# Optimization experiments

Measured on AMD Instinct MI355X. Metric: run time of the kernel, lower is better.

Reference implementation:

```python
import jax, jax.numpy as jnp
import numpy as np

N, E = 100000, 1600000
EPS = 1e-5  # BatchNorm1d default eps


def setup_inputs() -> dict:
    key = jax.random.key(0)
    ks = jax.random.split(key, 12)
    rn = lambda k, s, sc=0.05: jax.random.normal(k, s, dtype=jnp.float32) * sc
    return {
        "x": rn(ks[0], (N, 4), 1.0),
        "edge_attr": rn(ks[1], (E, 1), 1.0),
        "edge_index": jax.random.randint(ks[2], (2, E), 0, N),
        # Meta1 edge model: NNConv(9 -> 84) acting as a per-edge linear, + BN(84)
        "W_e1": rn(ks[3], (9, 84)), "b_e1": jnp.zeros((84,), jnp.float32),
        "g_bn1": jnp.ones((84,), jnp.float32), "be_bn1": jnp.zeros((84,), jnp.float32),
        # Meta1 node model: NNConv(88 -> 128) + BN(128), then Linear(132, 64)
        "W_n1": rn(ks[4], (88, 128)), "b_n1": jnp.zeros((128,), jnp.float32),
        "g_bn2": jnp.ones((128,), jnp.float32), "be_bn2": jnp.zeros((128,), jnp.float32),
        "W_m2": rn(ks[5], (132, 64)), "b_m2": jnp.zeros((64,), jnp.float32),
        # Meta2 edge model: Linear(212, 1)
        "W_e2": rn(ks[6], (212, 1)), "b_e2": jnp.zeros((1,), jnp.float32),
        # Meta2 node model: Linear(65, 4) (output discarded by the module)
        "W_n2": rn(ks[7], (65, 4)), "b_n2": jnp.zeros((4,), jnp.float32),
    }


def _batchnorm(h, g, b):
    # training-mode BatchNorm1d: batch mean / biased batch var
    m = jnp.mean(h, axis=0)
    v = jnp.mean(jnp.square(h - m), axis=0)
    return (h - m) * jax.lax.rsqrt(v + EPS) * g + b


def _scatter_mean(vals, idx, n):
    s = jax.ops.segment_sum(vals, idx, num_segments=n)
    cnt = jax.ops.segment_sum(jnp.ones((vals.shape[0],), vals.dtype), idx, num_segments=n)
    return s / jnp.maximum(cnt, 1.0)[:, None]


def reference(x, edge_attr, edge_index, W_e1, b_e1, g_bn1, be_bn1,
              W_n1, b_n1, g_bn2, be_bn2, W_m2, b_m2, W_e2, b_e2, W_n2, b_n2):
    row, col = edge_index[0], edge_index[1]
    n = x.shape[0]
    # --- Meta layer 1 ---
    # edge model: cat([src, dest, edge_attr]) -> NNConv(9,84) -> BN(84)
    e_in = jnp.concatenate([x[row], x[col], edge_attr], axis=1)            # [E, 9]
    e1 = _batchnorm(e_in @ W_e1 + b_e1, g_bn1, be_bn1)                     # [E, 84]
    # node model 1: gather + linear + BN + scatter_mean + concat + MLP
    h = jnp.concatenate([x[col], e1], axis=1) @ W_n1 + b_n1                # [E, 128]
    h = _batchnorm(h, g_bn2, be_bn2)
    agg = _scatter_mean(h, row, n)                                         # [N, 128]
    x1 = jax.nn.relu(jnp.concatenate([x, agg], axis=1) @ W_m2 + b_m2)      # [N, 64]
    # --- Meta layer 2 ---
    e2 = jax.nn.relu(
        jnp.concatenate([x1[row], x1[col], e1], axis=1) @ W_e2 + b_e2)     # [E, 1]
    # node model 2 is computed by the torch module but its output is discarded
    h2 = jax.nn.relu(jnp.concatenate([x1[col], e2], axis=1) @ W_n2 + b_n2)  # [E, 4]
    _x2 = jnp.concatenate([x1, _scatter_mean(h2, row, n)], axis=1)         # dead code
    return e2
```

## Files before the change

### kernel.cpp

```cpp
#include <hip/hip_runtime.h>


#define NBLK_A 512
#define CAPB 24
#define SHIFTB 7
#define SUBB 128
#define STGCAP 2048
#define M21 0x1FFFFFULL
#define QS2 2048.0f
#define QB2 16384

__global__ __launch_bounds__(1024) void k_passA(
    const int* __restrict__ ei, const float* __restrict__ ea,
    int2* __restrict__ rec, int* __restrict__ len,
    int NB, int E, int EPB)
{
    __shared__ int hist[1024];
    int t = threadIdx.x;
    int blk = blockIdx.x;
    if (t < 1024) hist[t] = 0;
    __syncthreads();
    int e0 = blk * EPB;
    int e1 = min(E, e0 + EPB);
    size_t base = (size_t)blk * NB;
    for (int e = e0 + t; e < e1; e += 1024) {
        int r = ei[e];
        int c = ei[E + e];
        float a = ea[e];
        int b = r >> SHIFTB;
        int slot = atomicAdd(&hist[b], 1);
        if (slot < CAPB) {
            int w0 = c | ((r & (SUBB - 1)) << 17);
            rec[(base + b) * CAPB + slot] = make_int2(w0, __float_as_int(a));
        }
    }
    __syncthreads();
    if (t < NB) len[base + t] = min(hist[t], CAPB);
}

__global__ __launch_bounds__(256) void k_passBR(
    const int2* __restrict__ rec, const int* __restrict__ len,
    const float4* __restrict__ x4, float* __restrict__ MSx,
    float* __restrict__ Tp, float* __restrict__ Up, int N, int NB)
{
    __shared__ unsigned long long Sacc[SUBB * 2];
    __shared__ int pre[257];
    __shared__ int wtot[4];
    __shared__ int2 stg[STGCAP];
    __shared__ float redT[40];
    __shared__ float redU[16];
    int t = threadIdx.x;
    int b = blockIdx.x;
    int w = t >> 6;
    int lane = t & 63;
    for (int k = t; k < SUBB * 2; k += 256) Sacc[k] = 0ULL;
    if (t < 40) redT[t] = 0.f;
    if (t < 16) redU[t] = 0.f;
    float u[15];
#pragma unroll
    for (int k = 0; k < 15; ++k) u[k] = 0.f;
    __syncthreads();
#pragma unroll
    for (int r = 0; r < NBLK_A / 256; ++r) {
        int seg = r * 256 + t;
        int lv = min(len[(size_t)seg * NB + b], CAPB);
        int v = lv;
#pragma unroll
        for (int off = 1; off < 64; off <<= 1) {
            int s = __shfl_up(v, off);
            if (lane >= off) v += s;
        }
        if (lane == 63) wtot[w] = v;
        __syncthreads();
        int wadd = 0;
#pragma unroll
        for (int k = 0; k < 4; ++k)
            if (k < w) wadd += wtot[k];
        pre[t + 1] = v + wadd;
        if (t == 0) pre[0] = 0;
        __syncthreads();
        int R = min(pre[256], STGCAP);
        int beg = pre[t + 1] - lv;
        const int2* sp = &rec[((size_t)seg * NB + b) * CAPB];
        for (int i = 0; i < lv; ++i) {
            int d = beg + i;
            if (d < STGCAP) stg[d] = sp[i];
        }
        __syncthreads();
#pragma unroll 4
        for (int idx = t; idx < R; idx += 256) {
            int2 v2 = stg[idx];
            int c = v2.x & 0x1FFFF;
            int ridx = v2.x >> 17;
            float a = __int_as_float(v2.y);
            float4 xc = x4[c];
            int q0 = __float2int_rn(xc.x * QS2);
            int q1 = __float2int_rn(xc.y * QS2);
            int q2 = __float2int_rn(xc.z * QS2);
            int q3 = __float2int_rn(xc.w * QS2);
            int qa = __float2int_rn(a * QS2);
            q0 = min(max(q0, -16383), 16383);
            q1 = min(max(q1, -16383), 16383);
            q2 = min(max(q2, -16383), 16383);
            q3 = min(max(q3, -16383), 16383);
            qa = min(max(qa, -16383), 16383);
            unsigned long long w0 =
                (unsigned long long)(unsigned)(q0 + QB2) |
                ((unsigned long long)(unsigned)(q1 + QB2) << 21) |
                ((unsigned long long)(unsigned)(q2 + QB2) << 42);
            unsigned long long w1 =
                (unsigned long long)(unsigned)(q3 + QB2) |
                ((unsigned long long)(unsigned)(qa + QB2) << 21) |
                (1ULL << 42);
            atomicAdd(&Sacc[ridx * 2], w0);
            atomicAdd(&Sacc[ridx * 2 + 1], w1);
            float zc[4] = {xc.x, xc.y, xc.z, xc.w};
            int q = 0;
#pragma unroll
            for (int i = 0; i < 4; ++i)
#pragma unroll
                for (int k = i; k < 4; ++k) { u[q] = fmaf(zc[i], zc[k], u[q]); ++q; }
#pragma unroll
            for (int i = 0; i < 4; ++i) u[10 + i] = fmaf(zc[i], a, u[10 + i]);
            u[14] = fmaf(a, a, u[14]);
        }
        __syncthreads();
    }
    float Tacc[39];
#pragma unroll
    for (int k = 0; k < 39; ++k) Tacc[k] = 0.f;
    int n = b * SUBB + t;
    if (t < SUBB && n < N) {
        unsigned long long w0 = Sacc[t * 2];
        unsigned long long w1 = Sacc[t * 2 + 1];
        long long f0 = (long long)(w0 & M21);
        long long f1 = (long long)((w0 >> 21) & M21);
        long long f2 = (long long)((w0 >> 42) & M21);
        long long f3 = (long long)(w1 & M21);
        long long fa = (long long)((w1 >> 21) & M21);
        long long cn = (long long)(w1 >> 42);
        float cnt = (float)cn;
        long long bias = cn * (long long)QB2;
        float S[6];
        S[0] = (float)(f0 - bias) / QS2;
        S[1] = (float)(f1 - bias) / QS2;
        S[2] = (float)(f2 - bias) / QS2;
        S[3] = (float)(f3 - bias) / QS2;
        S[4] = (float)(fa - bias) / QS2;
        S[5] = cnt;
        float4 xn = x4[n];
        float x[4] = {xn.x, xn.y, xn.z, xn.w};
        int q = 0;
#pragma unroll
        for (int a = 0; a < 4; ++a)
#pragma unroll
            for (int bb = a; bb < 4; ++bb) { Tacc[q] = cnt * x[a] * x[bb]; ++q; }
#pragma unroll
        for (int a = 0; a < 4; ++a)
#pragma unroll
            for (int bb = 0; bb < 4; ++bb) Tacc[10 + a * 4 + bb] = x[a] * S[bb];
#pragma unroll
        for (int a = 0; a < 4; ++a) {
            Tacc[26 + a] = x[a] * S[4];
            Tacc[30 + a] = cnt * x[a];
            Tacc[34 + a] = S[a];
        }
        Tacc[38] = S[4];
        float inv = cnt > 0.f ? 1.f / cnt : 0.f;
        float4* m = (float4*)(MSx + (size_t)n * 8);
        m[0] = make_float4(S[0] * inv, S[1] * inv, S[2] * inv, S[3] * inv);
        m[1] = make_float4(S[4] * inv, cnt > 0.f ? 1.f : 0.f, 0.f, 0.f);
    }
#pragma unroll
    for (int v = 0; v < 39; ++v) {
        float s = Tacc[v];
#pragma unroll
        for (int off = 32; off > 0; off >>= 1) s += __shfl_down(s, off);
        if (lane == 0) atomicAdd(&redT[v], s);
    }
#pragma unroll
    for (int v = 0; v < 15; ++v) {
        float s = u[v];
#pragma unroll
        for (int off = 32; off > 0; off >>= 1) s += __shfl_down(s, off);
        if (lane == 0) atomicAdd(&redU[v], s);
    }
    __syncthreads();
    if (t < 39) Tp[(size_t)b * 40 + t] = redT[t];
    else if (t >= 64 && t < 79) Up[(size_t)b * 16 + (t - 64)] = redU[t - 64];
}

__device__ __forceinline__ int sym4(int a, int b) {
    return a * 4 - a * (a - 1) / 2 + (b - a);
}

__global__ __launch_bounds__(1024) void k_setup(
    const float* __restrict__ Up, const float* __restrict__ Tp,
    int NBu, int NTb,
    const float* __restrict__ We1, const float* __restrict__ be1,
    const float* __restrict__ g1, const float* __restrict__ bb1,
    const float* __restrict__ Wn1, const float* __restrict__ bn1,
    const float* __restrict__ g2, const float* __restrict__ bb2,
    const float* __restrict__ We2, const float* __restrict__ be2,
    const float* __restrict__ Wm2, const float* __restrict__ bm2,
    float* __restrict__ G, float* __restrict__ c0g, float* __restrict__ kvg,
    int E)
{
    __shared__ float ZCl[64];
    __shared__ float Zf[100];
    __shared__ float s1[84], sh1[84];
    __shared__ float Ml[10 * 128];
    __shared__ float s2l[128], sh2l[128];
    __shared__ float Ep[16 * 64 * 11];
    __shared__ float We1l[9 * 84];
    __shared__ __align__(16) float Wn1l[88 * 128];
    __shared__ __align__(16) float Wm2l[132 * 64];
    __shared__ float We2l[212];
    __shared__ float be1l[84], g1l[84], bb1l[84];
    __shared__ float bn1l[128], g2l[128], bb2l[128];
    __shared__ float bm2l[64], be2l[1];
    int t = threadIdx.x;
    int lane = t & 63;
    if (t < 64) ZCl[t] = 0.f;
    {
        const float4* s4 = (const float4*)Wn1;
        float4* d4 = (float4*)Wn1l;
        for (int i = t; i < 88 * 128 / 4; i += 1024) d4[i] = s4[i];
        const float4* s5 = (const float4*)Wm2;
        float4* d5 = (float4*)Wm2l;
        for (int i = t; i < 132 * 64 / 4; i += 1024) d5[i] = s5[i];
        for (int i = t; i < 9 * 84; i += 1024) We1l[i] = We1[i];
        if (t < 212) We2l[t] = We2[t];
        if (t < 84) { be1l[t] = be1[t]; g1l[t] = g1[t]; bb1l[t] = bb1[t]; }
        else if (t >= 128 && t < 256) {
            int i = t - 128;
            bn1l[i] = bn1[i]; g2l[i] = g2[i]; bb2l[i] = bb2[i];
        } else if (t >= 256 && t < 320) bm2l[t - 256] = bm2[t - 256];
        if (t == 320) be2l[0] = be2[0];
    }
    float us[15];
#pragma unroll
    for (int k = 0; k < 15; ++k) us[k] = 0.f;
    for (int i = t; i < NBu; i += 1024)
#pragma unroll
        for (int k = 0; k < 15; ++k) us[k] += Up[(size_t)i * 16 + k];
    float ts[39];
#pragma unroll
    for (int k = 0; k < 39; ++k) ts[k] = 0.f;
    for (int i = t; i < NTb; i += 1024)
#pragma unroll
        for (int k = 0; k < 39; ++k) ts[k] += Tp[(size_t)i * 40 + k];
    __syncthreads();
#pragma unroll
    for (int v = 0; v < 15; ++v) {
        float s = us[v];
#pragma unroll
        for (int off = 32; off > 0; off >>= 1) s += __shfl_down(s, off);
        if (lane == 0) atomicAdd(&ZCl[39 + v], s);
    }
#pragma unroll
    for (int v = 0; v < 39; ++v) {
        float s = ts[v];
#pragma unroll
        for (int off = 32; off > 0; off >>= 1) s += __shfl_down(s, off);
        if (lane == 0) atomicAdd(&ZCl[v], s);
    }
    __syncthreads();
    if (t < 100) {
        int i = t / 10, jj = t % 10;
        int a_ = i < jj ? i : jj;
        int b_ = i < jj ? jj : i;
        float v;
        if (b_ < 4) v = ZCl[sym4(a_, b_)];
        else if (b_ < 8) {
            if (a_ < 4) v = ZCl[10 + a_ * 4 + (b_ - 4)];
            else v = ZCl[39 + sym4(a_ - 4, b_ - 4)];
        } else if (b_ == 8) {
            if (a_ < 4) v = ZCl[26 + a_];
            else if (a_ < 8) v = ZCl[49 + (a_ - 4)];
            else v = ZCl[53];
        } else {
            if (a_ < 4) v = ZCl[30 + a_];
            else if (a_ < 8) v = ZCl[34 + (a_ - 4)];
            else if (a_ == 8) v = ZCl[38];
            else v = (float)E;
        }
        Zf[t] = v;
    }
    __syncthreads();
    float Ef = (float)E;
    if (t < 84) {
        float w[10];
#pragma unroll
        for (int i = 0; i < 9; ++i) w[i] = We1l[i * 84 + t];
        w[9] = be1l[t];
        float sm = 0.f, sq = 0.f;
#pragma unroll
        for (int i = 0; i < 10; ++i) {
            sm += Zf[90 + i] * w[i];
            float zi = 0.f;
#pragma unroll
            for (int jj = 0; jj < 10; ++jj) zi += Zf[i * 10 + jj] * w[jj];
            sq += w[i] * zi;
        }
        float m = sm / Ef;
        float var = sq / Ef - m * m;
        float sc = g1l[t] * rsqrtf(var + 1e-5f);
        s1[t] = sc;
        sh1[t] = bb1l[t] - m * sc;
    }
    __syncthreads();
    {
        int j = t & 127;
        int sub = t >> 7;
        float col[10];
#pragma unroll
        for (int i = 0; i < 10; ++i) col[i] = 0.f;
        int k0 = sub * 11;
        int k1 = min(84, k0 + 11);
        for (int k = k0; k < k1; ++k) {
            float wn = Wn1l[(4 + k) * 128 + j];
            float ws_ = s1[k] * wn;
#pragma unroll
            for (int i = 0; i < 9; ++i) col[i] = fmaf(We1l[i * 84 + k], ws_, col[i]);
            col[9] += be1l[k] * ws_ + sh1[k] * wn;
        }
        float* bp = &Ep[(size_t)(sub * 128 + j) * 10];
#pragma unroll
        for (int i = 0; i < 10; ++i) bp[i] = col[i];
    }
    __syncthreads();
    if (t < 128) {
        float col[10];
#pragma unroll
        for (int i = 0; i < 10; ++i) col[i] = 0.f;
        for (int sub = 0; sub < 8; ++sub) {
            const float* bp = &Ep[(size_t)(sub * 128 + t) * 10];
#pragma unroll
            for (int i = 0; i < 10; ++i) col[i] += bp[i];
        }
#pragma unroll
        for (int i = 0; i < 4; ++i) col[4 + i] += Wn1l[i * 128 + t];
        col[9] += bn1l[t];
#pragma unroll
        for (int i = 0; i < 10; ++i) Ml[i * 128 + t] = col[i];
    }
    __syncthreads();
    if (t < 128) {
        float col[10];
#pragma unroll
        for (int i = 0; i < 10; ++i) col[i] = Ml[i * 128 + t];
        float sm = 0.f, sq = 0.f;
#pragma unroll
        for (int i = 0; i < 10; ++i) {
            sm += Zf[90 + i] * col[i];
            float zi = 0.f;
#pragma unroll
            for (int jj = 0; jj < 10; ++jj) zi += Zf[i * 10 + jj] * col[jj];
            sq += col[i] * zi;
        }
        float m = sm / Ef;
        float var = sq / Ef - m * m;
        float sc = g2l[t] * rsqrtf(var + 1e-5f);
        s2l[t] = sc;
        sh2l[t] = bb2l[t] - m * sc;
    } else if (t >= 128 && t < 768) {
        int col = (t - 128) >> 6;
        float kv = 0.f;
        if (col < 9) {
            for (int k = lane; k < 84; k += 64)
                kv = fmaf(We1l[col * 84 + k] * s1[k], We2l[128 + k], kv);
        } else {
            for (int k = lane; k < 84; k += 64)
                kv = fmaf(be1l[k] * s1[k] + sh1[k], We2l[128 + k], kv);
        }
#pragma unroll
        for (int off = 32; off > 0; off >>= 1) kv += __shfl_down(kv, off);
        if (lane == 0) kvg[col] = kv + (col == 9 ? be2l[0] : 0.f);
    }
    __syncthreads();
    {
        int j = t & 63;
        int sub = t >> 6;
        float gcol[10];
#pragma unroll
        for (int i = 0; i < 10; ++i) gcol[i] = 0.f;
        float c0 = 0.f;
        int k0 = sub * 8;
        for (int k = k0; k < k0 + 8; ++k) {
            float bkj = Wm2l[(4 + k) * 64 + j];
            float m = s2l[k] * bkj;
#pragma unroll
            for (int i = 0; i < 10; ++i) gcol[i] = fmaf(Ml[i * 128 + k], m, gcol[i]);
            c0 = fmaf(sh2l[k], bkj, c0);
        }
        float* ep = &Ep[(size_t)(sub * 64 + j) * 11];
#pragma unroll
        for (int i = 0; i < 10; ++i) ep[i] = gcol[i];
        ep[10] = c0;
    }
    __syncthreads();
    if (t < 64) {
        float gcol[10];
#pragma unroll
        for (int i = 0; i < 10; ++i) gcol[i] = 0.f;
        float c0 = 0.f;
        for (int sub = 0; sub < 16; ++sub) {
            const float* ep = &Ep[(size_t)(sub * 64 + t) * 11];
#pragma unroll
            for (int i = 0; i < 10; ++i) gcol[i] += ep[i];
            c0 += ep[10];
        }
#pragma unroll
        for (int i = 0; i < 4; ++i) gcol[i] += Wm2l[i * 64 + t];
        c0 += bm2l[t];
#pragma unroll
        for (int i = 0; i < 10; ++i) G[i * 64 + t] = gcol[i];
        c0g[t] = c0;
    }
}

__global__ __launch_bounds__(256) void k_nodesB(
    const float4* __restrict__ x4, const float* __restrict__ MSx,
    const float* __restrict__ G, const float* __restrict__ c0g,
    const float* __restrict__ kv, const float* __restrict__ Wm2,
    const float* __restrict__ bm2, const float* __restrict__ We2,
    float* __restrict__ P, float* __restrict__ Q, int N)
{
    __shared__ float Gl[640], c0l[64], Al[256], bl[64], ul[64], vl[64], kvl[10];
    int t = threadIdx.x;
    for (int k = t; k < 640; k += 256) Gl[k] = G[k];
    if (t < 64) {
        c0l[t] = c0g[t];
        bl[t] = bm2[t];
        ul[t] = We2[t];
        vl[t] = We2[64 + t];
    }
    for (int k = t; k < 256; k += 256) Al[k] = Wm2[k];
    if (t < 10) kvl[t] = kv[t];
    __syncthreads();
    int n = blockIdx.x * 256 + t;
    if (n >= N) return;
    float4 xn = x4[n];
    const float4* m = (const float4*)(MSx + (size_t)n * 8);
    float4 m0 = m[0];
    float4 m1 = m[1];
    bool has = m1.y > 0.5f;
    float Pv = 0.f, Qv = 0.f;
    if (has) {
        float zb[10] = {xn.x, xn.y, xn.z, xn.w, m0.x, m0.y, m0.z, m0.w, m1.x, 1.f};
#pragma unroll 4
        for (int j = 0; j < 64; ++j) {
            float s = c0l[j];
#pragma unroll
            for (int i = 0; i < 10; ++i) s = fmaf(zb[i], Gl[i * 64 + j], s);
            s = fmaxf(s, 0.f);
            Pv = fmaf(s, ul[j], Pv);
            Qv = fmaf(s, vl[j], Qv);
        }
    } else {
#pragma unroll 4
        for (int j = 0; j < 64; ++j) {
            float s = bl[j] + xn.x * Al[j] + xn.y * Al[64 + j] +
                      xn.z * Al[128 + j] + xn.w * Al[192 + j];
            s = fmaxf(s, 0.f);
            Pv = fmaf(s, ul[j], Pv);
            Qv = fmaf(s, vl[j], Qv);
        }
    }
    P[n] = Pv + xn.x * kvl[0] + xn.y * kvl[1] + xn.z * kvl[2] + xn.w * kvl[3];
    Q[n] = Qv + xn.x * kvl[4] + xn.y * kvl[5] + xn.z * kvl[6] + xn.w * kvl[7];
}

__global__ __launch_bounds__(256) void k_edges_out(
    const int* __restrict__ ei, const float* __restrict__ ea,
    const float* __restrict__ P, const float* __restrict__ Q,
    const float* __restrict__ kv, float* __restrict__ out, int E)
{
    int e4 = blockIdx.x * 256 + threadIdx.x;
    int e = e4 * 4;
    float k8 = kv[8], k9 = kv[9];
    if (e + 3 < E) {
        int4 rr = *(const int4*)&ei[e];
        int4 cc = *(const int4*)&ei[E + e];
        float4 aa = *(const float4*)&ea[e];
        float4 o;
        o.x = fmaxf(P[rr.x] + Q[cc.x] + aa.x * k8 + k9, 0.f);
        o.y = fmaxf(P[rr.y] + Q[cc.y] + aa.y * k8 + k9, 0.f);
        o.z = fmaxf(P[rr.z] + Q[cc.z] + aa.z * k8 + k9, 0.f);
        o.w = fmaxf(P[rr.w] + Q[cc.w] + aa.w * k8 + k9, 0.f);
        *(float4*)&out[e] = o;
    } else {
        for (; e < E; ++e) {
            float s = P[ei[e]] + Q[ei[E + e]] + ea[e] * k8 + k9;
            out[e] = fmaxf(s, 0.f);
        }
    }
}

extern "C" void kernel_launch(void* const* d_in, const int* in_sizes, int n_in,
                              void* d_out, int out_size, void* d_ws, size_t ws_size,
                              hipStream_t stream)
{
    const float* x   = (const float*)d_in[0];
    const float* ea  = (const float*)d_in[1];
    const int*   ei  = (const int*)d_in[2];
    const float* We1 = (const float*)d_in[3];
    const float* be1 = (const float*)d_in[4];
    const float* g1  = (const float*)d_in[5];
    const float* bb1 = (const float*)d_in[6];
    const float* Wn1 = (const float*)d_in[7];
    const float* bn1 = (const float*)d_in[8];
    const float* g2  = (const float*)d_in[9];
    const float* bb2 = (const float*)d_in[10];
    const float* Wm2 = (const float*)d_in[11];
    const float* bm2 = (const float*)d_in[12];
    const float* We2 = (const float*)d_in[13];
    const float* be2 = (const float*)d_in[14];

    int N = in_sizes[0] / 4;
    int E = in_sizes[1];
    int EPB = (E + NBLK_A - 1) / NBLK_A;

    int NB = (N + SUBB - 1) >> SHIFTB;

    float* ws  = (float*)d_ws;
    float* G   = ws + 64;
    float* c0  = ws + 704;
    float* kv  = ws + 768;
    float* P   = ws + 1024;
    float* Q   = P + N;
    float* MSx = Q + N;
    int*   len = (int*)(MSx + 8 * (size_t)N);
    int2*  rec = (int2*)(len + (size_t)NBLK_A * NB);

    float* Up = P;
    float* Tp = P + 32768;

    k_passA<<<NBLK_A, 1024, 0, stream>>>(ei, ea, rec, len, NB, E, EPB);
    k_passBR<<<NB, 256, 0, stream>>>(rec, len, (const float4*)x, MSx, Tp, Up,
                                     N, NB);
    k_setup<<<1, 1024, 0, stream>>>(Up, Tp, NB, NB, We1, be1, g1, bb1, Wn1,
                                    bn1, g2, bb2, We2, be2, Wm2, bm2, G, c0,
                                    kv, E);
    k_nodesB<<<(N + 255) / 256, 256, 0, stream>>>((const float4*)x, MSx, G,
                                                  c0, kv, Wm2, bm2, We2, P, Q,
                                                  N);
    k_edges_out<<<(E / 4 + 256) / 256, 256, 0, stream>>>(ei, ea, P, Q, kv,
                                                         (float*)d_out, E);
}
```

Measured before the change: 117.6 us.

## Transpose bucket lengths and stage all segments in one 512-thread pass

A new transpose kernel rewrites the per-segment bucket length table into bucket-major order, so each passBR block reads its 512 lengths contiguously. passBR now runs 512 threads per block and scans and stages all segments in a single round instead of two, which removes a round of barriers and prefix sums. The staging buffer grows to 2560 entries and records are read two at a time with int4 loads. In exchange this adds an extra kernel launch and raises shared memory use, and buckets whose total exceeds the larger staging cap would drop edges.

```diff
diff --git a/kernel.cpp b/kernel.cpp
--- a/kernel.cpp
+++ b/kernel.cpp
@@ -5,7 +5,7 @@
 #define CAPB 24
 #define SHIFTB 7
 #define SUBB 128
-#define STGCAP 2048
+#define STGCAP 2560
 #define M21 0x1FFFFFULL
 #define QS2 2048.0f
 #define QB2 16384
@@ -38,14 +38,33 @@
     if (t < NB) len[base + t] = min(hist[t], CAPB);
 }
 
-__global__ __launch_bounds__(256) void k_passBR(
-    const int2* __restrict__ rec, const int* __restrict__ len,
+__global__ __launch_bounds__(256) void k_transpose(
+    const int* __restrict__ in, int* __restrict__ out, int cols)
+{
+    __shared__ int tile[32][33];
+    int bx = blockIdx.x * 32;
+    int by = blockIdx.y * 32;
+    int tx = threadIdx.x & 31;
+    int ty0 = threadIdx.x >> 5;
+    for (int ty = ty0; ty < 32; ty += 8) {
+        int c = bx + tx;
+        tile[ty][tx] = (c < cols) ? in[(by + ty) * cols + c] : 0;
+    }
+    __syncthreads();
+    for (int ty = ty0; ty < 32; ty += 8) {
+        int b = bx + ty;
+        if (b < cols) out[(size_t)b * NBLK_A + (by + tx)] = tile[tx][ty];
+    }
+}
+
+__global__ __launch_bounds__(512) void k_passBR(
+    const int2* __restrict__ rec, const int* __restrict__ lenT,
     const float4* __restrict__ x4, float* __restrict__ MSx,
     float* __restrict__ Tp, float* __restrict__ Up, int N, int NB)
 {
     __shared__ unsigned long long Sacc[SUBB * 2];
-    __shared__ int pre[257];
-    __shared__ int wtot[4];
+    __shared__ int pre[513];
+    __shared__ int wtot[8];
     __shared__ int2 stg[STGCAP];
     __shared__ float redT[40];
     __shared__ float redU[16];
@@ -53,79 +72,79 @@
     int b = blockIdx.x;
     int w = t >> 6;
     int lane = t & 63;
-    for (int k = t; k < SUBB * 2; k += 256) Sacc[k] = 0ULL;
+    for (int k = t; k < SUBB * 2; k += 512) Sacc[k] = 0ULL;
     if (t < 40) redT[t] = 0.f;
     if (t < 16) redU[t] = 0.f;
     float u[15];
 #pragma unroll
     for (int k = 0; k < 15; ++k) u[k] = 0.f;
-    __syncthreads();
-#pragma unroll
-    for (int r = 0; r < NBLK_A / 256; ++r) {
-        int seg = r * 256 + t;
-        int lv = min(len[(size_t)seg * NB + b], CAPB);
-        int v = lv;
-#pragma unroll
-        for (int off = 1; off < 64; off <<= 1) {
-            int s = __shfl_up(v, off);
-            if (lane >= off) v += s;
-        }
-        if (lane == 63) wtot[w] = v;
-        __syncthreads();
-        int wadd = 0;
-#pragma unroll
-        for (int k = 0; k < 4; ++k)
-            if (k < w) wadd += wtot[k];
-        pre[t + 1] = v + wadd;
-        if (t == 0) pre[0] = 0;
-        __syncthreads();
-        int R = min(pre[256], STGCAP);
+    int lv = min(lenT[(size_t)b * NBLK_A + t], CAPB);
+    int v = lv;
+#pragma unroll
+    for (int off = 1; off < 64; off <<= 1) {
+        int s = __shfl_up(v, off);
+        if (lane >= off) v += s;
+    }
+    if (lane == 63) wtot[w] = v;
+    __syncthreads();
+    int wadd = 0;
+#pragma unroll
+    for (int k = 0; k < 8; ++k)
+        if (k < w) wadd += wtot[k];
+    pre[t + 1] = v + wadd;
+    if (t == 0) pre[0] = 0;
+    __syncthreads();
+    int R = min(pre[512], STGCAP);
+    {
         int beg = pre[t + 1] - lv;
-        const int2* sp = &rec[((size_t)seg * NB + b) * CAPB];
-        for (int i = 0; i < lv; ++i) {
+        const int2* sp = &rec[((size_t)t * NB + b) * CAPB];
+        for (int i = 0; i < lv; i += 2) {
+            int4 two = *(const int4*)&sp[i];
             int d = beg + i;
-            if (d < STGCAP) stg[d] = sp[i];
-        }
-        __syncthreads();
+            if (d < STGCAP) stg[d] = make_int2(two.x, two.y);
+            if (i + 1 < lv && d + 1 < STGCAP)
+                stg[d + 1] = make_int2(two.z, two.w);
+        }
+    }
+    __syncthreads();
 #pragma unroll 4
-        for (int idx = t; idx < R; idx += 256) {
-            int2 v2 = stg[idx];
-            int c = v2.x & 0x1FFFF;
-            int ridx = v2.x >> 17;
-            float a = __int_as_float(v2.y);
-            float4 xc = x4[c];
-            int q0 = __float2int_rn(xc.x * QS2);
-            int q1 = __float2int_rn(xc.y * QS2);
-            int q2 = __float2int_rn(xc.z * QS2);
-            int q3 = __float2int_rn(xc.w * QS2);
-            int qa = __float2int_rn(a * QS2);
-            q0 = min(max(q0, -16383), 16383);
-            q1 = min(max(q1, -16383), 16383);
-            q2 = min(max(q2, -16383), 16383);
-            q3 = min(max(q3, -16383), 16383);
-            qa = min(max(qa, -16383), 16383);
-            unsigned long long w0 =
-                (unsigned long long)(unsigned)(q0 + QB2) |
-                ((unsigned long long)(unsigned)(q1 + QB2) << 21) |
-                ((unsigned long long)(unsigned)(q2 + QB2) << 42);
-            unsigned long long w1 =
-                (unsigned long long)(unsigned)(q3 + QB2) |
-                ((unsigned long long)(unsigned)(qa + QB2) << 21) |
-                (1ULL << 42);
-            atomicAdd(&Sacc[ridx * 2], w0);
-            atomicAdd(&Sacc[ridx * 2 + 1], w1);
-            float zc[4] = {xc.x, xc.y, xc.z, xc.w};
-            int q = 0;
-#pragma unroll
-            for (int i = 0; i < 4; ++i)
-#pragma unroll
-                for (int k = i; k < 4; ++k) { u[q] = fmaf(zc[i], zc[k], u[q]); ++q; }
-#pragma unroll
-            for (int i = 0; i < 4; ++i) u[10 + i] = fmaf(zc[i], a, u[10 + i]);
-            u[14] = fmaf(a, a, u[14]);
-        }
-        __syncthreads();
-    }
+    for (int idx = t; idx < R; idx += 512) {
+        int2 v2 = stg[idx];
+        int c = v2.x & 0x1FFFF;
+        int ridx = v2.x >> 17;
+        float a = __int_as_float(v2.y);
+        float4 xc = x4[c];
+        int q0 = __float2int_rn(xc.x * QS2);
+        int q1 = __float2int_rn(xc.y * QS2);
+        int q2 = __float2int_rn(xc.z * QS2);
+        int q3 = __float2int_rn(xc.w * QS2);
+        int qa = __float2int_rn(a * QS2);
+        q0 = min(max(q0, -16383), 16383);
+        q1 = min(max(q1, -16383), 16383);
+        q2 = min(max(q2, -16383), 16383);
+        q3 = min(max(q3, -16383), 16383);
+        qa = min(max(qa, -16383), 16383);
+        unsigned long long w0 =
+            (unsigned long long)(unsigned)(q0 + QB2) |
+            ((unsigned long long)(unsigned)(q1 + QB2) << 21) |
+            ((unsigned long long)(unsigned)(q2 + QB2) << 42);
+        unsigned long long w1 =
+            (unsigned long long)(unsigned)(q3 + QB2) |
+            ((unsigned long long)(unsigned)(qa + QB2) << 21) |
+            (1ULL << 42);
+        atomicAdd(&Sacc[ridx * 2], w0);
+        atomicAdd(&Sacc[ridx * 2 + 1], w1);
+        float zc[4] = {xc.x, xc.y, xc.z, xc.w};
+        int q = 0;
+#pragma unroll
+        for (int i = 0; i < 4; ++i)
+#pragma unroll
+            for (int k = i; k < 4; ++k) { u[q] = fmaf(zc[i], zc[k], u[q]); ++q; }
+#pragma unroll
+        for (int i = 0; i < 4; ++i) u[10 + i] = fmaf(zc[i], a, u[10 + i]);
+        u[14] = fmaf(a, a, u[14]);
+    }
+    __syncthreads();
     float Tacc[39];
 #pragma unroll
     for (int k = 0; k < 39; ++k) Tacc[k] = 0.f;
@@ -172,18 +191,18 @@
         m[1] = make_float4(S[4] * inv, cnt > 0.f ? 1.f : 0.f, 0.f, 0.f);
     }
 #pragma unroll
-    for (int v = 0; v < 39; ++v) {
-        float s = Tacc[v];
+    for (int v2 = 0; v2 < 39; ++v2) {
+        float s = Tacc[v2];
 #pragma unroll
         for (int off = 32; off > 0; off >>= 1) s += __shfl_down(s, off);
-        if (lane == 0) atomicAdd(&redT[v], s);
-    }
-#pragma unroll
-    for (int v = 0; v < 15; ++v) {
-        float s = u[v];
+        if (lane == 0) atomicAdd(&redT[v2], s);
+    }
+#pragma unroll
+    for (int v2 = 0; v2 < 15; ++v2) {
+        float s = u[v2];
 #pragma unroll
         for (int off = 32; off > 0; off >>= 1) s += __shfl_down(s, off);
-        if (lane == 0) atomicAdd(&redU[v], s);
+        if (lane == 0) atomicAdd(&redU[v2], s);
     }
     __syncthreads();
     if (t < 39) Tp[(size_t)b * 40 + t] = redT[t];
@@ -532,13 +551,16 @@
     float* Q   = P + N;
     float* MSx = Q + N;
     int*   len = (int*)(MSx + 8 * (size_t)N);
-    int2*  rec = (int2*)(len + (size_t)NBLK_A * NB);
+    int*   lenT = len + (size_t)NBLK_A * NB;
+    int2*  rec = (int2*)(lenT + (size_t)NBLK_A * NB);
 
     float* Up = P;
     float* Tp = P + 32768;
 
     k_passA<<<NBLK_A, 1024, 0, stream>>>(ei, ea, rec, len, NB, E, EPB);
-    k_passBR<<<NB, 256, 0, stream>>>(rec, len, (const float4*)x, MSx, Tp, Up,
+    k_transpose<<<dim3((NB + 31) / 32, NBLK_A / 32), 256, 0, stream>>>(
+        len, lenT, NB);
+    k_passBR<<<NB, 512, 0, stream>>>(rec, lenT, (const float4*)x, MSx, Tp, Up,
                                      N, NB);
     k_setup<<<1, 1024, 0, stream>>>(Up, Tp, NB, NB, We1, be1, g1, bb1, Wn1,
                                     bn1, g2, bb2, We2, be2, Wm2, bm2, G, c0,
```

Result: slower. 136.1 us (+15.7%).
